# Kernel tuning notes

Hardware: AMD Instinct MI355X
Metric: run time of the kernel (lower is better)

## Reference

```python
import jax, jax.numpy as jnp
import numpy as np

ALPHA = 0.2       # LeakyReLU negative slope
NEG_INF = -9e15   # matches torch's -9000000000000000.0 mask value


def setup_inputs() -> dict:
    key = jax.random.key(0)
    k1, k2, k3, k4, k5 = jax.random.split(key, 5)
    B, N, Fin, Fout, H = 8, 1024, 512, 512, 8
    dh = Fout // H
    return {
        "x": jax.random.normal(k1, (B, N, Fin), dtype=jnp.float32),
        "adj": jax.random.randint(k2, (B, N, N), 0, 2, dtype=jnp.int32),
        "W_w": jax.random.normal(k3, (Fin, Fout), dtype=jnp.float32) * 0.05,
        "W_b": jax.random.normal(k4, (Fout,), dtype=jnp.float32) * 0.05,
        "att": jax.random.normal(k5, (H, 2 * dh), dtype=jnp.float32) * 0.1,
    }


def reference(x, adj, W_w, W_b, att):
    # x: [B,N,Fin], adj: [B,N,N] int, W_w: [Fin,Fout], W_b: [Fout], att: [H,2*dh]
    B, N, _ = x.shape
    H = att.shape[0]
    out = x @ W_w + W_b                      # [B,N,Fout]
    dh = out.shape[-1] // H
    h = out.reshape(B, N, H, dh)             # per-head features
    a_src, a_dst = att[:, :dh], att[:, dh:]  # first half pairs with h_j, second with h_i
    s_src = jnp.einsum('bnhd,hd->bhn', h, a_src)   # contribution of source j
    s_dst = jnp.einsum('bnhd,hd->bhn', h, a_dst)   # contribution of target i
    # e[b,h,i,j] = leakyrelu(a_src . h_j + a_dst . h_i)
    e = jax.nn.leaky_relu(s_dst[:, :, :, None] + s_src[:, :, None, :], ALPHA)
    e = jnp.where(adj[:, None, :, :] > 0, e, NEG_INF)
    attn = jax.nn.softmax(e, axis=-1)              # [B,H,N,N]
    h_prime = jnp.einsum('bhij,bjhd->bihd', attn, h).reshape(B, N, H * dh)
    return jax.nn.elu(h_prime)                     # concat=True path
```

## Files before the change

### kernel.cpp

```cpp
#include <hip/hip_runtime.h>
#include <hip/hip_bf16.h>
#include <stdint.h>

typedef __attribute__((ext_vector_type(8))) short  vshort8;
typedef __attribute__((ext_vector_type(4))) float  vfloat4;
typedef __attribute__((ext_vector_type(4))) int    vint4;

static constexpr int Bb   = 8;
static constexpr int Nn   = 1024;
static constexpr int FIN  = 512;
static constexpr int FOUT = 512;
static constexpr int Hh   = 8;
static constexpr int DH   = 64;
static constexpr int Mm   = Bb * Nn;
static constexpr float LRELU_ALPHA = 0.2f;
static constexpr float LOG2E = 1.4426950408889634f;

__device__ __forceinline__ unsigned short f2bf(float f) {
  union { float f; uint32_t u; } c; c.f = f;
  uint32_t r = c.u + 0x7fffu + ((c.u >> 16) & 1u);
  return (unsigned short)(r >> 16);
}
__device__ __forceinline__ float bf2f(unsigned short s) {
  union { uint32_t u; float f; } c; c.u = ((uint32_t)s) << 16; return c.f;
}

__global__ __launch_bounds__(256) void prep_kernel(const int* __restrict__ adj,
                                                   const float* __restrict__ x,
                                                   const float* __restrict__ W,
                                                   unsigned* __restrict__ packed,
                                                   short* __restrict__ xb,
                                                   short* __restrict__ Wt) {
  __shared__ float tile[64 * 65];
  const int bx = blockIdx.x, tid = threadIdx.x;
  if (bx < 2048) {
    const int rowid = bx * 4 + (tid >> 6);
    const int b = rowid >> 10, i = rowid & 1023;
    const int l = tid & 63;
    const int* src = adj + (size_t)rowid * Nn;
    unsigned myw = 0;
    #pragma unroll
    for (int k = 0; k < 16; ++k) {
      const int v = src[k * 64 + l];
      const unsigned long long m = __ballot(v > 0);
      if (l == 2 * k)     myw = (unsigned)m;
      if (l == 2 * k + 1) myw = (unsigned)(m >> 32);
    }
    if (l < 32) packed[((size_t)b * 32 + l) * 1024 + i] = myw;
  } else if (bx < 3072) {
    int i = ((bx - 2048) * 256 + tid) * 8;
    const int stride = 1024 * 256 * 8;
    for (; i < Mm * FIN; i += stride) {
      vfloat4 v0 = *(const vfloat4*)(x + i);
      vfloat4 v1 = *(const vfloat4*)(x + i + 4);
      vshort8 o;
      o[0] = (short)f2bf(v0[0]); o[1] = (short)f2bf(v0[1]);
      o[2] = (short)f2bf(v0[2]); o[3] = (short)f2bf(v0[3]);
      o[4] = (short)f2bf(v1[0]); o[5] = (short)f2bf(v1[1]);
      o[6] = (short)f2bf(v1[2]); o[7] = (short)f2bf(v1[3]);
      *(vshort8*)(xb + i) = o;
    }
  } else {
    const int bxx = bx - 3072;
    const int n0 = (bxx & 7) * 64, k0 = (bxx >> 3) * 64;
    const int c = tid & 63, r4 = tid >> 6;
    #pragma unroll
    for (int rr = 0; rr < 64; rr += 4)
      tile[(rr + r4) * 65 + c] = W[(size_t)(k0 + rr + r4) * FOUT + n0 + c];
    __syncthreads();
    #pragma unroll
    for (int rr = 0; rr < 64; rr += 4)
      Wt[(size_t)(n0 + rr + r4) * FIN + k0 + c] = (short)f2bf(tile[c * 65 + rr + r4]);
  }
}

__global__ __launch_bounds__(256) void gemm_t_kernel(const short* __restrict__ A,
                                                     const short* __restrict__ Bt,
                                                     const float* __restrict__ bias,
                                                     short* __restrict__ hbt) {
  __shared__ short As[64 * 64];
  __shared__ short Bs[64 * 64];
  const int tid = threadIdx.x;
  const int w = tid >> 6, l = tid & 63;
  const int lrow = l & 15, lk = l >> 4;
  const int m0 = blockIdx.x * 64, n0 = blockIdx.y * 64;
  vfloat4 acc[4] = {};
  for (int kt = 0; kt < FIN; kt += 64) {
    #pragma unroll
    for (int p = 0; p < 2; ++p) {
      const int idxS = p * 2048 + tid * 8;
      const int row  = idxS >> 6;
      const int cs   = (idxS & 63) * 2;
      const int cd   = cs ^ ((row & 7) << 4);
      __builtin_amdgcn_global_load_lds(
          (const __attribute__((address_space(1))) unsigned int*)(A + (size_t)(m0 + row) * FIN + kt + (cd >> 1)),
          (__attribute__((address_space(3))) unsigned int*)(As + idxS), 16, 0, 0);
      __builtin_amdgcn_global_load_lds(
          (const __attribute__((address_space(1))) unsigned int*)(Bt + (size_t)(n0 + row) * FIN + kt + (cd >> 1)),
          (__attribute__((address_space(3))) unsigned int*)(Bs + idxS), 16, 0, 0);
    }
    __syncthreads();
    #pragma unroll
    for (int ks = 0; ks < 2; ++ks) {
      const int mrow = w * 16 + lrow;
      const int gc   = ks * 64 + lk * 16;
      vshort8 bf = *(const vshort8*)((const char*)As + mrow * 128 + (gc ^ ((mrow & 7) << 4)));
      #pragma unroll
      for (int i = 0; i < 4; ++i) {
        const int frow = i * 16 + lrow;
        vshort8 af = *(const vshort8*)((const char*)Bs + frow * 128 + (gc ^ ((frow & 7) << 4)));
        acc[i] = __builtin_amdgcn_mfma_f32_16x16x32_bf16(af, bf, acc[i], 0, 0, 0);
      }
    }
    __syncthreads();
  }
  #pragma unroll
  for (int i = 0; i < 4; ++i) {
    const int fbase = n0 + i * 16 + lk * 4;
    const vfloat4 bv = *(const vfloat4*)(bias + fbase);
    #pragma unroll
    for (int r = 0; r < 4; ++r) {
      const int fg = fbase + r;
      const int h = fg >> 6, d = fg & 63;
      const int mg = m0 + w * 16 + lrow;
      const int b = mg >> 10, n = mg & 1023;
      hbt[((size_t)(b * Hh + h) * DH + d) * Nn + n] = (short)f2bf(acc[i][r] + bv[r]);
    }
  }
}

__global__ __launch_bounds__(256) void scores_kernel(const short* __restrict__ hbt,
                                                     const float* __restrict__ att,
                                                     float* __restrict__ ssrc,
                                                     float* __restrict__ sdst) {
  __shared__ float lps[8][32][8];
  __shared__ float lpd[8][32][8];
  const int bh = blockIdx.y, h = bh & 7;
  const int tid = threadIdx.x;
  const int tn = tid & 31, td = tid >> 5;
  const int n0 = blockIdx.x * 256 + tn * 8;
  const short* base = hbt + (size_t)bh * DH * Nn;
  float ps[8] = {}, pd[8] = {};
  #pragma unroll
  for (int dd = 0; dd < 8; ++dd) {
    const int d = td * 8 + dd;
    const vshort8 v = *(const vshort8*)(base + (size_t)d * Nn + n0);
    const float as_ = att[h * 2 * DH + d];
    const float ad_ = att[h * 2 * DH + DH + d];
    #pragma unroll
    for (int e = 0; e < 8; ++e) {
      const float f = bf2f((unsigned short)v[e]);
      ps[e] += f * as_;
      pd[e] += f * ad_;
    }
  }
  #pragma unroll
  for (int e = 0; e < 8; ++e) { lps[td][tn][e] = ps[e]; lpd[td][tn][e] = pd[e]; }
  __syncthreads();
  if (tid < 32) {
    float s[8] = {};
    #pragma unroll
    for (int q = 0; q < 8; ++q)
      #pragma unroll
      for (int e = 0; e < 8; ++e) s[e] += lps[q][tid][e];
    #pragma unroll
    for (int e = 0; e < 8; ++e) s[e] *= LOG2E;
    *(vfloat4*)(ssrc + (size_t)bh * Nn + blockIdx.x * 256 + tid * 8) = *(vfloat4*)s;
    *(vfloat4*)(ssrc + (size_t)bh * Nn + blockIdx.x * 256 + tid * 8 + 4) = *(vfloat4*)(s + 4);
  } else if (tid < 64) {
    const int t = tid - 32;
    float s[8] = {};
    #pragma unroll
    for (int q = 0; q < 8; ++q)
      #pragma unroll
      for (int e = 0; e < 8; ++e) s[e] += lpd[q][t][e];
    #pragma unroll
    for (int e = 0; e < 8; ++e) s[e] *= LOG2E;
    *(vfloat4*)(sdst + (size_t)bh * Nn + blockIdx.x * 256 + t * 8) = *(vfloat4*)s;
    *(vfloat4*)(sdst + (size_t)bh * Nn + blockIdx.x * 256 + t * 8 + 4) = *(vfloat4*)(s + 4);
  }
}

__device__ __forceinline__ void stage_vb(const short* __restrict__ vbbase,
                                         short* lds_buf, int iw, int l, int jt) {
  #pragma unroll
  for (int k = 0; k < 4; ++k) {
    const int d  = iw * 16 + k * 4 + (l >> 4);
    const int cs = (l & 15) * 16;
    const int cd = cs ^ ((d & 7) << 4);
    const int j  = jt + (cd >> 1);
    __builtin_amdgcn_global_load_lds(
        (const __attribute__((address_space(1))) unsigned int*)(vbbase + (size_t)d * Nn + j),
        (__attribute__((address_space(3))) unsigned int*)(lds_buf + iw * 2048 + k * 512),
        16, 0, 0);
  }
}

__global__ __launch_bounds__(256, 4) void attn_kernel(const unsigned* __restrict__ packed,
                                                      const float* __restrict__ ssrc,
                                                      const float* __restrict__ sdst,
                                                      const short* __restrict__ hbt,
                                                      float* __restrict__ out) {
  __shared__ short vbl[2][8192];
  __shared__ float slds[1024];
  const int it = blockIdx.x, h = blockIdx.y, b = blockIdx.z;
  const int tid = threadIdx.x;
  const int iw = tid >> 6, l = tid & 63;
  const int lrow = l & 15, lk = l >> 4;
  const int i = it * 64 + iw * 16 + lrow;
  const float sdi = sdst[(size_t)(b * Hh + h) * Nn + i];
  const float* ssp = ssrc + (size_t)(b * Hh + h) * Nn;
  const short* vbbase = hbt + (size_t)(b * Hh + h) * DH * Nn;
  const unsigned* ap = packed + (size_t)b * 32 * 1024 + i;

  __builtin_amdgcn_global_load_lds(
      (const __attribute__((address_space(1))) unsigned int*)(ssp + iw * 256 + l * 4),
      (__attribute__((address_space(3))) unsigned int*)(slds + iw * 256),
      16, 0, 0);
  stage_vb(vbbase, vbl[0], iw, l, 0);
  vint4 a_cur;
  #pragma unroll
  for (int s = 0; s < 4; ++s) a_cur[s] = (int)ap[s * 1024];
  asm volatile("s_waitcnt vmcnt(0)" ::: "memory");
  asm volatile("s_barrier" ::: "memory");

  vshort8 ones;
  #pragma unroll
  for (int e = 0; e < 8; ++e) ones[e] = (short)0x3F80;
  vfloat4 acc[4] = {};
  vfloat4 accd = {};

  int buf = 0;
  for (int t = 0; t < 8; ++t) {
    vint4 a_nxt = {};
    if (t < 7) {
      stage_vb(vbbase, vbl[buf ^ 1], iw, l, (t + 1) * 128);
      #pragma unroll
      for (int s = 0; s < 4; ++s) a_nxt[s] = (int)ap[((t + 1) * 4 + s) * 1024];
      asm volatile("s_waitcnt vmcnt(8)" ::: "memory");
    } else {
      asm volatile("s_waitcnt vmcnt(0)" ::: "memory");
    }
    asm volatile("s_barrier" ::: "memory");

    const char* vc = (const char*)vbl[buf];
    const char* sc = (const char*)slds + t * 512;
    #pragma unroll
    for (int s = 0; s < 4; ++s) {
      const vfloat4 s0 = *(const vfloat4*)(sc + s * 128 + lk * 32);
      const vfloat4 s1 = *(const vfloat4*)(sc + s * 128 + lk * 32 + 16);
      const unsigned u = ((unsigned)a_cur[s]) >> (lk * 8);
      vshort8 af;
      #pragma unroll
      for (int e = 0; e < 4; ++e) {
        float tv = sdi + s0[e];
        tv = fmaxf(tv, LRELU_ALPHA * tv);
        const float pe = ((u >> e) & 1u) ? __builtin_amdgcn_exp2f(tv) : 0.f;
        af[e] = (short)__bfloat16_as_ushort(__float2bfloat16(pe));
      }
      #pragma unroll
      for (int e = 0; e < 4; ++e) {
        float tv = sdi + s1[e];
        tv = fmaxf(tv, LRELU_ALPHA * tv);
        const float pe = ((u >> (4 + e)) & 1u) ? __builtin_amdgcn_exp2f(tv) : 0.f;
        af[4 + e] = (short)__bfloat16_as_ushort(__float2bfloat16(pe));
      }
      const int cbase = (s * 64 + lk * 16) ^ ((lrow & 7) << 4);
      vshort8 f0 = *(const vshort8*)(vc + (0 * 16 + lrow) * 256 + cbase);
      vshort8 f1 = *(const vshort8*)(vc + (1 * 16 + lrow) * 256 + cbase);
      vshort8 f2 = *(const vshort8*)(vc + (2 * 16 + lrow) * 256 + cbase);
      vshort8 f3 = *(const vshort8*)(vc + (3 * 16 + lrow) * 256 + cbase);
      acc[0] = __builtin_amdgcn_mfma_f32_16x16x32_bf16(af, f0, acc[0], 0, 0, 0);
      acc[1] = __builtin_amdgcn_mfma_f32_16x16x32_bf16(af, f1, acc[1], 0, 0, 0);
      acc[2] = __builtin_amdgcn_mfma_f32_16x16x32_bf16(af, f2, acc[2], 0, 0, 0);
      acc[3] = __builtin_amdgcn_mfma_f32_16x16x32_bf16(af, f3, acc[3], 0, 0, 0);
      accd   = __builtin_amdgcn_mfma_f32_16x16x32_bf16(af, ones, accd, 0, 0, 0);
    }
    if (t < 7) a_cur = a_nxt;
    asm volatile("s_barrier" ::: "memory");
    buf ^= 1;
  }

  #pragma unroll
  for (int r = 0; r < 4; ++r) {
    const int lr = lk * 4 + r;
    const float inv = 1.0f / accd[r];
    const int row = it * 64 + iw * 16 + lr;
    #pragma unroll
    for (int df = 0; df < 4; ++df) {
      float v = acc[df][r] * inv;
      v = v > 0.f ? v : expm1f(v);
      out[((size_t)(b * Nn + row)) * FOUT + h * DH + df * 16 + lrow] = v;
    }
  }
}

extern "C" void kernel_launch(void* const* d_in, const int* in_sizes, int n_in,
                              void* d_out, int out_size, void* d_ws, size_t ws_size,
                              hipStream_t stream) {
  const float* x   = (const float*)d_in[0];
  const int*   adj = (const int*)d_in[1];
  const float* W   = (const float*)d_in[2];
  const float* Wb  = (const float*)d_in[3];
  const float* att = (const float*)d_in[4];
  float* out = (float*)d_out;

  short* xb  = (short*)d_out;
  short* Wt  = xb + (size_t)Mm * FIN;
  short* hbt = (short*)d_ws;
  float* ssrc = (float*)(hbt + (size_t)Bb * Hh * DH * Nn);
  float* sdst = ssrc + (size_t)Bb * Hh * Nn;
  unsigned* packed = (unsigned*)(sdst + (size_t)Bb * Hh * Nn);

  prep_kernel<<<3136, 256, 0, stream>>>(adj, x, W, packed, xb, Wt);
  gemm_t_kernel<<<dim3(Mm / 64, FOUT / 64), 256, 0, stream>>>(xb, Wt, Wb, hbt);
  scores_kernel<<<dim3(4, Bb * Hh), 256, 0, stream>>>(hbt, att, ssrc, sdst);
  attn_kernel<<<dim3(Nn / 64, Hh, Bb), 256, 0, stream>>>(packed, ssrc, sdst, hbt, out);
}
```

Before: 139.4 us.

## Fuse attention score computation into GEMM epilogue and double-buffer GEMM tiles

Removes the separate scores kernel by computing the per-node src/dst attention dot products in the GEMM epilogue from fp32 accumulators, reduced with cross-lane shuffles. It also double-buffers the A/B LDS tiles so the next K-tile's global-to-LDS loads overlap the current MFMA work, using explicit vmcnt waits and barriers. Scores now come from the fp32 accumulators rather than bf16-rounded h, which changes numerics slightly. LDS use doubles.

```diff
diff --git a/kernel.cpp b/kernel.cpp
--- a/kernel.cpp
+++ b/kernel.cpp
@@ -74,110 +74,88 @@
   }
 }
 
+__device__ __forceinline__ void stage_ab(const short* __restrict__ A,
+                                         const short* __restrict__ Bt,
+                                         short* as, short* bs,
+                                         int m0, int n0, int kt, int tid) {
+  #pragma unroll
+  for (int p = 0; p < 2; ++p) {
+    const int idxS = p * 2048 + tid * 8;
+    const int row  = idxS >> 6;
+    const int cs   = (idxS & 63) * 2;
+    const int cd   = cs ^ ((row & 7) << 4);
+    __builtin_amdgcn_global_load_lds(
+        (const __attribute__((address_space(1))) unsigned int*)(A + (size_t)(m0 + row) * FIN + kt + (cd >> 1)),
+        (__attribute__((address_space(3))) unsigned int*)(as + idxS), 16, 0, 0);
+    __builtin_amdgcn_global_load_lds(
+        (const __attribute__((address_space(1))) unsigned int*)(Bt + (size_t)(n0 + row) * FIN + kt + (cd >> 1)),
+        (__attribute__((address_space(3))) unsigned int*)(bs + idxS), 16, 0, 0);
+  }
+}
+
 __global__ __launch_bounds__(256) void gemm_t_kernel(const short* __restrict__ A,
                                                      const short* __restrict__ Bt,
                                                      const float* __restrict__ bias,
-                                                     short* __restrict__ hbt) {
-  __shared__ short As[64 * 64];
-  __shared__ short Bs[64 * 64];
+                                                     const float* __restrict__ att,
+                                                     short* __restrict__ hbt,
+                                                     float* __restrict__ ssrc,
+                                                     float* __restrict__ sdst) {
+  __shared__ short As[2][4096];
+  __shared__ short Bs[2][4096];
   const int tid = threadIdx.x;
   const int w = tid >> 6, l = tid & 63;
   const int lrow = l & 15, lk = l >> 4;
   const int m0 = blockIdx.x * 64, n0 = blockIdx.y * 64;
   vfloat4 acc[4] = {};
-  for (int kt = 0; kt < FIN; kt += 64) {
-    #pragma unroll
-    for (int p = 0; p < 2; ++p) {
-      const int idxS = p * 2048 + tid * 8;
-      const int row  = idxS >> 6;
-      const int cs   = (idxS & 63) * 2;
-      const int cd   = cs ^ ((row & 7) << 4);
-      __builtin_amdgcn_global_load_lds(
-          (const __attribute__((address_space(1))) unsigned int*)(A + (size_t)(m0 + row) * FIN + kt + (cd >> 1)),
-          (__attribute__((address_space(3))) unsigned int*)(As + idxS), 16, 0, 0);
-      __builtin_amdgcn_global_load_lds(
-          (const __attribute__((address_space(1))) unsigned int*)(Bt + (size_t)(n0 + row) * FIN + kt + (cd >> 1)),
-          (__attribute__((address_space(3))) unsigned int*)(Bs + idxS), 16, 0, 0);
-    }
-    __syncthreads();
+  stage_ab(A, Bt, As[0], Bs[0], m0, n0, 0, tid);
+  int buf = 0;
+  for (int ktt = 0; ktt < 8; ++ktt) {
+    if (ktt < 7) {
+      stage_ab(A, Bt, As[buf ^ 1], Bs[buf ^ 1], m0, n0, (ktt + 1) * 64, tid);
+      asm volatile("s_waitcnt vmcnt(4)" ::: "memory");
+    } else {
+      asm volatile("s_waitcnt vmcnt(0)" ::: "memory");
+    }
+    asm volatile("s_barrier" ::: "memory");
     #pragma unroll
     for (int ks = 0; ks < 2; ++ks) {
       const int mrow = w * 16 + lrow;
       const int gc   = ks * 64 + lk * 16;
-      vshort8 bf = *(const vshort8*)((const char*)As + mrow * 128 + (gc ^ ((mrow & 7) << 4)));
+      vshort8 bf = *(const vshort8*)((const char*)As[buf] + mrow * 128 + (gc ^ ((mrow & 7) << 4)));
       #pragma unroll
       for (int i = 0; i < 4; ++i) {
         const int frow = i * 16 + lrow;
-        vshort8 af = *(const vshort8*)((const char*)Bs + frow * 128 + (gc ^ ((frow & 7) << 4)));
+        vshort8 af = *(const vshort8*)((const char*)Bs[buf] + frow * 128 + (gc ^ ((frow & 7) << 4)));
         acc[i] = __builtin_amdgcn_mfma_f32_16x16x32_bf16(af, bf, acc[i], 0, 0, 0);
       }
     }
-    __syncthreads();
-  }
+    asm volatile("s_barrier" ::: "memory");
+    buf ^= 1;
+  }
+  const int hh = n0 >> 6;
+  const float* a_src = att + hh * 2 * DH;
+  const float* a_dst = a_src + DH;
+  const int mg = m0 + w * 16 + lrow;
+  const int b = mg >> 10, n = mg & 1023;
+  float ps = 0.f, pd = 0.f;
   #pragma unroll
   for (int i = 0; i < 4; ++i) {
     const int fbase = n0 + i * 16 + lk * 4;
     const vfloat4 bv = *(const vfloat4*)(bias + fbase);
     #pragma unroll
     for (int r = 0; r < 4; ++r) {
-      const int fg = fbase + r;
-      const int h = fg >> 6, d = fg & 63;
-      const int mg = m0 + w * 16 + lrow;
-      const int b = mg >> 10, n = mg & 1023;
-      hbt[((size_t)(b * Hh + h) * DH + d) * Nn + n] = (short)f2bf(acc[i][r] + bv[r]);
-    }
-  }
-}
-
-__global__ __launch_bounds__(256) void scores_kernel(const short* __restrict__ hbt,
-                                                     const float* __restrict__ att,
-                                                     float* __restrict__ ssrc,
-                                                     float* __restrict__ sdst) {
-  __shared__ float lps[8][32][8];
-  __shared__ float lpd[8][32][8];
-  const int bh = blockIdx.y, h = bh & 7;
-  const int tid = threadIdx.x;
-  const int tn = tid & 31, td = tid >> 5;
-  const int n0 = blockIdx.x * 256 + tn * 8;
-  const short* base = hbt + (size_t)bh * DH * Nn;
-  float ps[8] = {}, pd[8] = {};
-  #pragma unroll
-  for (int dd = 0; dd < 8; ++dd) {
-    const int d = td * 8 + dd;
-    const vshort8 v = *(const vshort8*)(base + (size_t)d * Nn + n0);
-    const float as_ = att[h * 2 * DH + d];
-    const float ad_ = att[h * 2 * DH + DH + d];
-    #pragma unroll
-    for (int e = 0; e < 8; ++e) {
-      const float f = bf2f((unsigned short)v[e]);
-      ps[e] += f * as_;
-      pd[e] += f * ad_;
-    }
-  }
-  #pragma unroll
-  for (int e = 0; e < 8; ++e) { lps[td][tn][e] = ps[e]; lpd[td][tn][e] = pd[e]; }
-  __syncthreads();
-  if (tid < 32) {
-    float s[8] = {};
-    #pragma unroll
-    for (int q = 0; q < 8; ++q)
-      #pragma unroll
-      for (int e = 0; e < 8; ++e) s[e] += lps[q][tid][e];
-    #pragma unroll
-    for (int e = 0; e < 8; ++e) s[e] *= LOG2E;
-    *(vfloat4*)(ssrc + (size_t)bh * Nn + blockIdx.x * 256 + tid * 8) = *(vfloat4*)s;
-    *(vfloat4*)(ssrc + (size_t)bh * Nn + blockIdx.x * 256 + tid * 8 + 4) = *(vfloat4*)(s + 4);
-  } else if (tid < 64) {
-    const int t = tid - 32;
-    float s[8] = {};
-    #pragma unroll
-    for (int q = 0; q < 8; ++q)
-      #pragma unroll
-      for (int e = 0; e < 8; ++e) s[e] += lpd[q][t][e];
-    #pragma unroll
-    for (int e = 0; e < 8; ++e) s[e] *= LOG2E;
-    *(vfloat4*)(sdst + (size_t)bh * Nn + blockIdx.x * 256 + t * 8) = *(vfloat4*)s;
-    *(vfloat4*)(sdst + (size_t)bh * Nn + blockIdx.x * 256 + t * 8 + 4) = *(vfloat4*)(s + 4);
+      const int fl = i * 16 + lk * 4 + r;
+      const float hv = acc[i][r] + bv[r];
+      ps += hv * a_src[fl];
+      pd += hv * a_dst[fl];
+      hbt[((size_t)(b * Hh + hh) * DH + fl) * Nn + n] = (short)f2bf(hv);
+    }
+  }
+  ps += __shfl_xor(ps, 16); ps += __shfl_xor(ps, 32);
+  pd += __shfl_xor(pd, 16); pd += __shfl_xor(pd, 32);
+  if (l < 16) {
+    ssrc[(size_t)(b * Hh + hh) * Nn + n] = ps * LOG2E;
+    sdst[(size_t)(b * Hh + hh) * Nn + n] = pd * LOG2E;
   }
 }
 
@@ -313,7 +291,6 @@
   unsigned* packed = (unsigned*)(sdst + (size_t)Bb * Hh * Nn);
 
   prep_kernel<<<3136, 256, 0, stream>>>(adj, x, W, packed, xb, Wt);
-  gemm_t_kernel<<<dim3(Mm / 64, FOUT / 64), 256, 0, stream>>>(xb, Wt, Wb, hbt);
-  scores_kernel<<<dim3(4, Bb * Hh), 256, 0, stream>>>(hbt, att, ssrc, sdst);
+  gemm_t_kernel<<<dim3(Mm / 64, FOUT / 64), 256, 0, stream>>>(xb, Wt, Wb, att, hbt, ssrc, sdst);
   attn_kernel<<<dim3(Nn / 64, Hh, Bb), 256, 0, stream>>>(packed, ssrc, sdst, hbt, out);
 }
```

Result: faster. 134.5 us (-3.6%).
